# Performance work log

Measured on AMD Instinct MI355X. Metric: run time of the kernel, lower is better.

The kernel has to match this reference:

```python
import jax, jax.numpy as jnp
import numpy as np

K = 3        # kernel_size
S = 1        # stride
P = 1        # padding
SCALE = 1000.0  # scale_factor
SUMMARY = 'avg'


def _unfold(x, k, s, p):
    # torch.nn.functional.unfold: (N,C,H,W) -> (N, C*k*k, L), channel-major then (kh,kw)
    N, C, H, W = x.shape
    Hout = (H + 2 * p - k) // s + 1
    Wout = (W + 2 * p - k) // s + 1
    xp = jnp.pad(x, ((0, 0), (0, 0), (p, p), (p, p)))
    cols = [xp[:, :, ki:ki + s * Hout:s, kj:kj + s * Wout:s]
            for ki in range(k) for kj in range(k)]
    patches = jnp.stack(cols, axis=2)  # (N, C, k*k, Hout, Wout)
    return patches.reshape(N, C * k * k, Hout * Wout), Hout, Wout


def _rep_first(s):
    # For each position l, index of the FIRST position j with s[j] == s[l].
    # Equivalent to unique(return_index, return_inverse): ui[di[l]].
    L = s.shape[0]
    order = jnp.argsort(s)                 # stable sort (jax default)
    ss = s[order]
    is_new = jnp.concatenate([jnp.ones((1,), bool), ss[1:] != ss[:-1]])
    pos = jnp.where(is_new, jnp.arange(L), 0)
    last_new = jax.lax.cummax(pos)         # position (in sorted order) of current group start
    rep_sorted = order[last_new]           # first-occurrence original index per group
    return jnp.zeros(L, jnp.int32).at[order].set(rep_sorted.astype(jnp.int32))


def setup_inputs() -> dict:
    key = jax.random.key(0)
    k1, k2, k3 = jax.random.split(key, 3)
    fmap = jax.random.normal(k1, (8, 64, 128, 128), dtype=jnp.float32)
    weight = jax.random.normal(k2, (128, 576), dtype=jnp.float32) * 0.05
    bias = jax.random.normal(k3, (128, 1), dtype=jnp.float32) * 0.05
    return {"fmap": fmap, "weight": weight, "bias": bias}


def reference(fmap, weight, bias):
    cols, Hout, Wout = _unfold(fmap, K, S, P)          # (N, Cin*K*K, L)
    if SUMMARY == 'avg':
        summ = cols.mean(axis=1)                        # (N, L)
    else:
        summ = cols.max(axis=1)
    summ = (summ * SCALE).astype(jnp.int32)             # trunc toward zero, like .int()
    rep = jax.vmap(_rep_first)(summ)                    # (N, L) representative patch index
    gathered = jnp.take_along_axis(cols, rep[:, None, :], axis=2)  # (N, P, L)
    out = jnp.einsum('op,npl->nol', weight, gathered) + bias[None]  # (N, Cout, L)
    N = fmap.shape[0]
    return out.reshape(N, weight.shape[0], Hout, Wout)
```

## Files before the change

kernel.cpp:

```cpp
#include <hip/hip_runtime.h>
#include <stdint.h>

#define NIMG 8
#define CIN 64
#define HH 128
#define WWID 128
#define L (HH*WWID)
#define COUT 128
#define PATCH 576
#define TBL 65536
#define OFFV 32768
#define CAP 4096
#define SPB 8

__global__ __launch_bounds__(256) void csum_kernel(const float* __restrict__ fmap,
                                                   double* __restrict__ csum) {
    int idx = blockIdx.x * blockDim.x + threadIdx.x;
    if (idx >= NIMG * L / 4) return;
    int n   = idx >> 12;
    int hw4 = (idx & (L / 4 - 1)) << 2;
    const float* p = fmap + (size_t)n * CIN * L + hw4;
    double s0 = 0, s1 = 0, s2 = 0, s3 = 0;
    #pragma unroll 8
    for (int c = 0; c < CIN; ++c) {
        float4 v = *(const float4*)(p + (size_t)c * L);
        s0 += (double)v.x; s1 += (double)v.y; s2 += (double)v.z; s3 += (double)v.w;
    }
    double* q = csum + (size_t)n * L + hw4;
    q[0] = s0; q[1] = s1; q[2] = s2; q[3] = s3;
}

__global__ void quant_kernel(const double* __restrict__ csum, int* __restrict__ qarr,
                             unsigned int* __restrict__ firstIdx) {
    int idx = blockIdx.x * blockDim.x + threadIdx.x;
    if (idx >= NIMG * L) return;
    int n  = idx >> 14;
    int hw = idx & (L - 1);
    int h = hw >> 7, w = hw & 127;
    const double* base = csum + (size_t)n * L;
    double s = 0.0;
    #pragma unroll
    for (int ki = -1; ki <= 1; ++ki) {
        int hh = h + ki;
        if (hh < 0 || hh >= HH) continue;
        #pragma unroll
        for (int kj = -1; kj <= 1; ++kj) {
            int ww = w + kj;
            if (ww < 0 || ww >= WWID) continue;
            s += base[hh * WWID + ww];
        }
    }
    double avg = s / 576.0;
    int q = (int)(avg * 1000.0);
    qarr[idx] = q;
    int v = q + OFFV;
    v = v < 0 ? 0 : (v > TBL - 1 ? TBL - 1 : v);
    atomicMin(&firstIdx[(size_t)n * TBL + v], (unsigned int)hw);
}

__global__ void compact_kernel(const unsigned int* __restrict__ firstIdx,
                               int* __restrict__ slotTab, unsigned int* __restrict__ uniqJ,
                               int* __restrict__ count) {
    int idx = blockIdx.x * blockDim.x + threadIdx.x;
    if (idx >= NIMG * TBL) return;
    unsigned int fi = firstIdx[idx];
    if (fi != 0xFFFFFFFFu) {
        int n = idx >> 16;
        int s = atomicAdd(&count[n], 1);
        slotTab[idx] = s;
        if (s < CAP) uniqJ[n * CAP + s] = fi;
    }
}

__global__ __launch_bounds__(256) void gemm_kernel(const float* __restrict__ fmap,
                            const float* __restrict__ weight, const float* __restrict__ bias,
                            const unsigned int* __restrict__ uniqJ, const int* __restrict__ count,
                            float* __restrict__ R) {
    int n  = blockIdx.y;
    int s0 = blockIdx.x * SPB;
    int cnt = count[n];
    if (cnt > CAP) cnt = CAP;
    if (s0 >= cnt) return;

    __shared__ float patch[SPB][PATCH];
    __shared__ float part[COUT][SPB + 1];
    int tid = threadIdx.x;

    #pragma unroll
    for (int i = tid; i < SPB * PATCH; i += 256) {
        int si = i / PATCH, p = i - si * PATCH;
        float v = 0.f;
        int s = s0 + si;
        if (s < cnt) {
            unsigned int j = uniqJ[n * CAP + s];
            int h0 = j >> 7, w0 = j & 127;
            int c = p / 9, r = p - c * 9;
            int hh = h0 + r / 3 - 1;
            int ww = w0 + (r % 3) - 1;
            if (hh >= 0 && hh < HH && ww >= 0 && ww < WWID)
                v = fmap[((size_t)n * CIN + c) * L + hh * WWID + ww];
        }
        patch[si][p] = v;
    }
    __syncthreads();

    int o     = tid & 127;
    int half  = tid >> 7;
    int kbase = half * (PATCH / 2);
    const float* wrow = weight + (size_t)o * PATCH + kbase;

    float acc[SPB];
    #pragma unroll
    for (int i = 0; i < SPB; ++i) acc[i] = 0.f;

    #pragma unroll 4
    for (int kk = 0; kk < PATCH / 2; kk += 4) {
        float4 wv = *(const float4*)(wrow + kk);
        #pragma unroll
        for (int i = 0; i < SPB; ++i) {
            float4 pv = *(const float4*)(&patch[i][kbase + kk]);
            acc[i] += wv.x * pv.x + wv.y * pv.y + wv.z * pv.z + wv.w * pv.w;
        }
    }

    if (half == 1) {
        #pragma unroll
        for (int i = 0; i < SPB; ++i) part[o][i] = acc[i];
    }
    __syncthreads();
    if (half == 0) {
        float b = bias[o];
        float* Rrow = R + ((size_t)n * COUT + o) * CAP;
        #pragma unroll
        for (int i = 0; i < SPB; ++i) {
            int s = s0 + i;
            if (s < cnt) Rrow[s] = acc[i] + part[o][i] + b;
        }
    }
}

__global__ __launch_bounds__(256) void scatter_kernel(const float* __restrict__ weight,
                               const float* __restrict__ bias, const float* __restrict__ fmap,
                               const int* __restrict__ qarr, const int* __restrict__ slotTab,
                               const unsigned int* __restrict__ firstIdx,
                               const float* __restrict__ R, float* __restrict__ out) {
    int idx = blockIdx.x * blockDim.x + threadIdx.x;
    if (idx >= NIMG * COUT * L / 4) return;
    int l4 = (idx & (L / 4 - 1)) << 2;
    int o  = (idx >> 12) & 127;
    int n  = idx >> 19;

    int4 q4 = *(const int4*)(qarr + (size_t)n * L + l4);
    const int* st = slotTab + (size_t)n * TBL;
    const float* Rrow = R + ((size_t)n * COUT + o) * CAP;

    float4 val;
    float* vp = (float*)&val;
    const int* qp = (const int*)&q4;
    #pragma unroll
    for (int e = 0; e < 4; ++e) {
        int q = qp[e];
        int v = q + OFFV;
        v = v < 0 ? 0 : (v > TBL - 1 ? TBL - 1 : v);
        int s = st[v];
        if (s < CAP) {
            vp[e] = Rrow[s];
        } else {
            unsigned int j = firstIdx[(size_t)n * TBL + v];
            int h0 = j >> 7, w0 = j & 127;
            const float* wr = weight + (size_t)o * PATCH;
            float acc = 0.f;
            for (int c = 0; c < CIN; ++c)
                for (int r = 0; r < 9; ++r) {
                    int hh = h0 + r / 3 - 1;
                    int ww = w0 + (r % 3) - 1;
                    float pv = (hh >= 0 && hh < HH && ww >= 0 && ww < WWID)
                               ? fmap[((size_t)n * CIN + c) * L + hh * WWID + ww] : 0.f;
                    acc += wr[c * 9 + r] * pv;
                }
            vp[e] = acc + bias[o];
        }
    }
    *(float4*)(out + ((size_t)n * COUT + o) * L + l4) = val;
}

extern "C" void kernel_launch(void* const* d_in, const int* in_sizes, int n_in,
                              void* d_out, int out_size, void* d_ws, size_t ws_size,
                              hipStream_t stream) {
    const float* fmap   = (const float*)d_in[0];
    const float* weight = (const float*)d_in[1];
    const float* bias   = (const float*)d_in[2];
    float* out = (float*)d_out;

    char* ws = (char*)d_ws;
    double*       csum     = (double*)ws;        ws += (size_t)NIMG * L * 8;
    int*          qarr     = (int*)ws;           ws += (size_t)NIMG * L * 4;
    unsigned int* firstIdx = (unsigned int*)ws;  ws += (size_t)NIMG * TBL * 4;
    int*          slotTab  = (int*)ws;           ws += (size_t)NIMG * TBL * 4;
    unsigned int* uniqJ    = (unsigned int*)ws;  ws += (size_t)NIMG * CAP * 4;
    int*          count    = (int*)ws;           ws += 128;
    float*        R        = (float*)ws;         ws += (size_t)NIMG * COUT * CAP * 4;

    hipMemsetAsync(firstIdx, 0xFF, (size_t)NIMG * TBL * 4, stream);
    hipMemsetAsync(count, 0, 128, stream);

    int nl4 = NIMG * L / 4;
    csum_kernel <<<(nl4 + 255) / 256, 256, 0, stream>>>(fmap, csum);
    quant_kernel<<<(NIMG * L + 255) / 256, 256, 0, stream>>>(csum, qarr, firstIdx);
    compact_kernel<<<(NIMG * TBL + 255) / 256, 256, 0, stream>>>(firstIdx, slotTab, uniqJ, count);
    dim3 gg(CAP / SPB, NIMG);
    gemm_kernel<<<gg, 256, 0, stream>>>(fmap, weight, bias, uniqJ, count, R);
    int no4 = NIMG * COUT * L / 4;
    scatter_kernel<<<(no4 + 255) / 256, 256, 0, stream>>>(weight, bias, fmap, qarr, slotTab, firstIdx, R, out);
}
```

Measured before the change: 213.8 us.

## Fuse channel-sum and quantize into tiled kernel; transpose weights for GEMM

Merges the channel-sum and 3x3-window quantization kernels into one tiled kernel that keeps 18x18 double channel sums in shared memory. This removes the global double csum buffer and one launch, at the cost of recomputing halo sums and doing scalar rather than float4 loads. The GEMM now reads a transposed weight copy, built each call by a new kernel. Each thread computes two output channels over a quarter of K, with a four-way shared-memory reduction.

```diff
diff --git a/kernel.cpp b/kernel.cpp
--- a/kernel.cpp
+++ b/kernel.cpp
@@ -13,46 +13,50 @@
 #define CAP 4096
 #define SPB 8
 
-__global__ __launch_bounds__(256) void csum_kernel(const float* __restrict__ fmap,
-                                                   double* __restrict__ csum) {
-    int idx = blockIdx.x * blockDim.x + threadIdx.x;
-    if (idx >= NIMG * L / 4) return;
-    int n   = idx >> 12;
-    int hw4 = (idx & (L / 4 - 1)) << 2;
-    const float* p = fmap + (size_t)n * CIN * L + hw4;
-    double s0 = 0, s1 = 0, s2 = 0, s3 = 0;
-    #pragma unroll 8
-    for (int c = 0; c < CIN; ++c) {
-        float4 v = *(const float4*)(p + (size_t)c * L);
-        s0 += (double)v.x; s1 += (double)v.y; s2 += (double)v.z; s3 += (double)v.w;
-    }
-    double* q = csum + (size_t)n * L + hw4;
-    q[0] = s0; q[1] = s1; q[2] = s2; q[3] = s3;
-}
-
-__global__ void quant_kernel(const double* __restrict__ csum, int* __restrict__ qarr,
-                             unsigned int* __restrict__ firstIdx) {
-    int idx = blockIdx.x * blockDim.x + threadIdx.x;
-    if (idx >= NIMG * L) return;
-    int n  = idx >> 14;
-    int hw = idx & (L - 1);
-    int h = hw >> 7, w = hw & 127;
-    const double* base = csum + (size_t)n * L;
+__global__ __launch_bounds__(256) void wtrans_kernel(const float* __restrict__ W,
+                                                     float* __restrict__ Wt) {
+    int idx = blockIdx.x * 256 + threadIdx.x;
+    if (idx >= COUT * PATCH) return;
+    int k = idx >> 7, o = idx & 127;
+    Wt[idx] = W[o * PATCH + k];
+}
+
+__global__ __launch_bounds__(256) void csq_kernel(const float* __restrict__ fmap,
+                                                  int* __restrict__ qarr,
+                                                  unsigned int* __restrict__ firstIdx) {
+    int bid  = blockIdx.x;
+    int n    = bid >> 6;
+    int tile = bid & 63;
+    int h0 = (tile >> 3) << 4;
+    int w0 = (tile & 7) << 4;
+    __shared__ double cs[18 * 18];
+    int tid = threadIdx.x;
+    const float* fb = fmap + (size_t)n * CIN * L;
+
+    for (int p = tid; p < 324; p += 256) {
+        int th = p / 18, tw = p - th * 18;
+        int h = h0 + th - 1, w = w0 + tw - 1;
+        double s = 0.0;
+        if (h >= 0 && h < HH && w >= 0 && w < WWID) {
+            const float* q = fb + h * WWID + w;
+            #pragma unroll 8
+            for (int c = 0; c < CIN; ++c) s += (double)q[(size_t)c * L];
+        }
+        cs[p] = s;
+    }
+    __syncthreads();
+
+    int th = tid >> 4, tw = tid & 15;
     double s = 0.0;
     #pragma unroll
-    for (int ki = -1; ki <= 1; ++ki) {
-        int hh = h + ki;
-        if (hh < 0 || hh >= HH) continue;
-        #pragma unroll
-        for (int kj = -1; kj <= 1; ++kj) {
-            int ww = w + kj;
-            if (ww < 0 || ww >= WWID) continue;
-            s += base[hh * WWID + ww];
-        }
-    }
+    for (int ki = 0; ki < 3; ++ki)
+        #pragma unroll
+        for (int kj = 0; kj < 3; ++kj)
+            s += cs[(th + ki) * 18 + tw + kj];
     double avg = s / 576.0;
     int q = (int)(avg * 1000.0);
-    qarr[idx] = q;
+    int hw = (h0 + th) * WWID + (w0 + tw);
+    qarr[n * L + hw] = q;
     int v = q + OFFV;
     v = v < 0 ? 0 : (v > TBL - 1 ? TBL - 1 : v);
     atomicMin(&firstIdx[(size_t)n * TBL + v], (unsigned int)hw);
@@ -73,7 +77,7 @@
 }
 
 __global__ __launch_bounds__(256) void gemm_kernel(const float* __restrict__ fmap,
-                            const float* __restrict__ weight, const float* __restrict__ bias,
+                            const float* __restrict__ Wt, const float* __restrict__ bias,
                             const unsigned int* __restrict__ uniqJ, const int* __restrict__ count,
                             float* __restrict__ R) {
     int n  = blockIdx.y;
@@ -83,7 +87,7 @@
     if (s0 >= cnt) return;
 
     __shared__ float patch[SPB][PATCH];
-    __shared__ float part[COUT][SPB + 1];
+    __shared__ float part[3][64][2][SPB];
     int tid = threadIdx.x;
 
     #pragma unroll
@@ -93,10 +97,10 @@
         int s = s0 + si;
         if (s < cnt) {
             unsigned int j = uniqJ[n * CAP + s];
-            int h0 = j >> 7, w0 = j & 127;
+            int hj = j >> 7, wj = j & 127;
             int c = p / 9, r = p - c * 9;
-            int hh = h0 + r / 3 - 1;
-            int ww = w0 + (r % 3) - 1;
+            int hh = hj + r / 3 - 1;
+            int ww = wj + (r % 3) - 1;
             if (hh >= 0 && hh < HH && ww >= 0 && ww < WWID)
                 v = fmap[((size_t)n * CIN + c) * L + hh * WWID + ww];
         }
@@ -104,37 +108,51 @@
     }
     __syncthreads();
 
-    int o     = tid & 127;
-    int half  = tid >> 7;
-    int kbase = half * (PATCH / 2);
-    const float* wrow = weight + (size_t)o * PATCH + kbase;
-
-    float acc[SPB];
-    #pragma unroll
-    for (int i = 0; i < SPB; ++i) acc[i] = 0.f;
-
-    #pragma unroll 4
-    for (int kk = 0; kk < PATCH / 2; kk += 4) {
-        float4 wv = *(const float4*)(wrow + kk);
+    int op = tid & 63;
+    int kq = tid >> 6;
+    int kbase = kq * (PATCH / 4);
+
+    float acc[2][SPB];
+    #pragma unroll
+    for (int j = 0; j < 2; ++j)
+        #pragma unroll
+        for (int i = 0; i < SPB; ++i) acc[j][i] = 0.f;
+
+    const float* wp = Wt + (size_t)kbase * COUT + op * 2;
+    #pragma unroll 2
+    for (int kk = 0; kk < PATCH / 4; kk += 4) {
+        float2 w0 = *(const float2*)(wp + (kk + 0) * COUT);
+        float2 w1 = *(const float2*)(wp + (kk + 1) * COUT);
+        float2 w2 = *(const float2*)(wp + (kk + 2) * COUT);
+        float2 w3 = *(const float2*)(wp + (kk + 3) * COUT);
         #pragma unroll
         for (int i = 0; i < SPB; ++i) {
             float4 pv = *(const float4*)(&patch[i][kbase + kk]);
-            acc[i] += wv.x * pv.x + wv.y * pv.y + wv.z * pv.z + wv.w * pv.w;
-        }
-    }
-
-    if (half == 1) {
-        #pragma unroll
-        for (int i = 0; i < SPB; ++i) part[o][i] = acc[i];
+            acc[0][i] += w0.x * pv.x + w1.x * pv.y + w2.x * pv.z + w3.x * pv.w;
+            acc[1][i] += w0.y * pv.x + w1.y * pv.y + w2.y * pv.z + w3.y * pv.w;
+        }
+    }
+
+    if (kq) {
+        #pragma unroll
+        for (int j = 0; j < 2; ++j)
+            #pragma unroll
+            for (int i = 0; i < SPB; ++i) part[kq - 1][op][j][i] = acc[j][i];
     }
     __syncthreads();
-    if (half == 0) {
-        float b = bias[o];
-        float* Rrow = R + ((size_t)n * COUT + o) * CAP;
-        #pragma unroll
-        for (int i = 0; i < SPB; ++i) {
-            int s = s0 + i;
-            if (s < cnt) Rrow[s] = acc[i] + part[o][i] + b;
+    if (kq == 0) {
+        #pragma unroll
+        for (int j = 0; j < 2; ++j) {
+            int o = op * 2 + j;
+            float b = bias[o];
+            float* Rrow = R + ((size_t)n * COUT + o) * CAP;
+            #pragma unroll
+            for (int i = 0; i < SPB; ++i) {
+                int s = s0 + i;
+                if (s < cnt)
+                    Rrow[s] = acc[j][i] + part[0][op][j][i] + part[1][op][j][i]
+                            + part[2][op][j][i] + b;
+            }
         }
     }
 }
@@ -193,23 +211,22 @@
     float* out = (float*)d_out;
 
     char* ws = (char*)d_ws;
-    double*       csum     = (double*)ws;        ws += (size_t)NIMG * L * 8;
     int*          qarr     = (int*)ws;           ws += (size_t)NIMG * L * 4;
     unsigned int* firstIdx = (unsigned int*)ws;  ws += (size_t)NIMG * TBL * 4;
     int*          slotTab  = (int*)ws;           ws += (size_t)NIMG * TBL * 4;
     unsigned int* uniqJ    = (unsigned int*)ws;  ws += (size_t)NIMG * CAP * 4;
     int*          count    = (int*)ws;           ws += 128;
+    float*        Wt       = (float*)ws;         ws += (size_t)COUT * PATCH * 4;
     float*        R        = (float*)ws;         ws += (size_t)NIMG * COUT * CAP * 4;
 
     hipMemsetAsync(firstIdx, 0xFF, (size_t)NIMG * TBL * 4, stream);
     hipMemsetAsync(count, 0, 128, stream);
 
-    int nl4 = NIMG * L / 4;
-    csum_kernel <<<(nl4 + 255) / 256, 256, 0, stream>>>(fmap, csum);
-    quant_kernel<<<(NIMG * L + 255) / 256, 256, 0, stream>>>(csum, qarr, firstIdx);
+    wtrans_kernel<<<(COUT * PATCH + 255) / 256, 256, 0, stream>>>(weight, Wt);
+    csq_kernel<<<NIMG * 64, 256, 0, stream>>>(fmap, qarr, firstIdx);
     compact_kernel<<<(NIMG * TBL + 255) / 256, 256, 0, stream>>>(firstIdx, slotTab, uniqJ, count);
     dim3 gg(CAP / SPB, NIMG);
-    gemm_kernel<<<gg, 256, 0, stream>>>(fmap, weight, bias, uniqJ, count, R);
+    gemm_kernel<<<gg, 256, 0, stream>>>(fmap, Wt, bias, uniqJ, count, R);
     int no4 = NIMG * COUT * L / 4;
     scatter_kernel<<<(no4 + 255) / 256, 256, 0, stream>>>(weight, bias, fmap, qarr, slotTab, firstIdx, R, out);
 }
```

Result: faster. 203.8 us (-4.7%).
